# Performance work log

Hardware: AMD Instinct MI355X
Metric: run time of the kernel (lower is better)

The kernel has to match this reference:

```python
import jax, jax.numpy as jnp
import numpy as np

IN, H, OUT = 8, 256, 24  # input_size, hidden_size, output_size
B, T = 2048, 256


def _gate_step(hx, x, Wx, Wh, b):
    # Fused version of the 8 per-gate Linears: one [.,IN]@[IN,4H] + one [.,H]@[H,4H]
    gates = x @ Wx + hx @ Wh + b            # [B, 4H]
    i, f, o, g = jnp.split(gates, 4, axis=-1)
    i, f, o = jax.nn.sigmoid(i), jax.nn.sigmoid(f), jax.nn.sigmoid(o)
    g = jnp.tanh(g)
    # NOTE: in the original code cx is never reassigned, so it stays zeros and
    # cy = cx*f + i*g == i*g on every step. We replicate that exactly.
    cy = i * g
    return o * jnp.tanh(cy)


def setup_inputs() -> dict:
    key = jax.random.key(0)
    ks = jax.random.split(key, 9)
    s = 0.05
    return {
        "inputs0": jax.random.normal(ks[0], (B, T, IN), jnp.float32),
        "inputs1": jax.random.normal(ks[1], (B, OUT - 1), jnp.float32),
        # concatenated gate weights, order [i | f | o | c]
        "Wx": jax.random.normal(ks[2], (IN, 4 * H), jnp.float32) * s,
        "Wh": jax.random.normal(ks[3], (H, 4 * H), jnp.float32) * s,
        "b": jax.random.normal(ks[4], (4 * H,), jnp.float32) * s,  # bx + bh folded
        "Wy": jax.random.normal(ks[5], (H, 1), jnp.float32) * s,
        "by": jax.random.normal(ks[6], (1,), jnp.float32) * s,
        # fresh random Linear(1, IN) per decoder step in the original -> per-step params
        "dec_w": jax.random.normal(ks[7], (OUT - 1, IN), jnp.float32) * s,
        "dec_b": jax.random.normal(ks[8], (OUT - 1, IN), jnp.float32) * s,
    }


def reference(inputs0, inputs1, Wx, Wh, b, Wy, by, dec_w, dec_b):
    bsz = inputs0.shape[0]
    h0 = jnp.zeros((bsz, H), inputs0.dtype)

    # ---- encoder: scan over time (strict recurrence) ----
    x_seq = jnp.transpose(inputs0, (1, 0, 2))  # [T, B, IN]

    def enc_step(h, x):
        return _gate_step(h, x, Wx, Wh, b), None

    h, _ = jax.lax.scan(enc_step, h0, x_seq)
    hy0 = h @ Wy + by                           # [B, 1]

    # ---- decoder: OUT-1 steps, each with its own fresh 1->IN linear ----
    x1_seq = jnp.transpose(inputs1, (1, 0))[: OUT - 1]  # [OUT-1, B]

    def dec_step(h, inp):
        x1, w, bb = inp
        x = x1[:, None] * w[None, :] + bb[None, :]      # [B, IN]
        h = _gate_step(h, x, Wx, Wh, b)
        return h, h @ Wy + by                            # y: [B, 1]

    _, ys = jax.lax.scan(dec_step, h, (x1_seq, dec_w, dec_b))  # ys: [OUT-1, B, 1]

    hy = jnp.concatenate([hy0, jnp.transpose(ys[..., 0], (1, 0))], axis=1)  # [B, OUT]
    return hy
```

## Files before the change

### kernel.cpp

```cpp
#include <hip/hip_runtime.h>


typedef short bf16x8 __attribute__((ext_vector_type(8)));
typedef float f32x4 __attribute__((ext_vector_type(4)));

#define T_ENC 256
#define N_DEC 23
#define NSTEP 279
#define HSTR 296
#define REG_T 37
#define LDS_T 17
#define WPACK_SHORTS (48 * 9 * 512)

__device__ __forceinline__ short f2bf(float f) {
  unsigned u = __float_as_uint(f);
  u = (u + 0x7fffu + ((u >> 16) & 1u)) >> 16;
  return (short)u;
}
__device__ __forceinline__ float bf2f(short s) {
  return __uint_as_float(((unsigned)(unsigned short)s) << 16);
}

#if __has_builtin(__builtin_amdgcn_rcpf)
#define RCPF(x) __builtin_amdgcn_rcpf(x)
#else
#define RCPF(x) (1.0f / (x))
#endif

__device__ __forceinline__ float sigm(float x) { return RCPF(1.0f + __expf(-x)); }
__device__ __forceinline__ float tanhf_fast(float x) {
  return 1.0f - 2.0f * RCPF(__expf(2.0f * x) + 1.0f);
}

__global__ void pack_kernel(const float* __restrict__ Wx, const float* __restrict__ Wh,
                            const float* __restrict__ b, short* __restrict__ Wpack,
                            float* __restrict__ bpack) {
  int tau = blockIdx.x;
  int l = threadIdx.x;
  int n_tile = tau / 9, kt = tau % 9;
  int w = n_tile / 6, t = n_tile % 6;
  int gate = t >> 1, loc = t & 1;
  int base = (gate == 0) ? 0 : (gate == 1 ? 512 : 768);
  int c = l & 15, q = l >> 4;
  int oc = base + w * 32 + loc * 16 + c;
  bf16x8 v;
#pragma unroll
  for (int e = 0; e < 8; ++e) {
    int k = kt * 32 + q * 8 + e;
    float f;
    if (k < 256)      f = Wh[k * 1024 + oc];
    else if (k < 264) f = Wx[(k - 256) * 1024 + oc];
    else              f = 0.0f;
    v[e] = f2bf(f);
  }
  ((bf16x8*)Wpack)[tau * 64 + l] = v;
  if (kt == 0 && q == 0) bpack[n_tile * 16 + c] = b[oc];
}

__global__ __launch_bounds__(512, 2) void lstm_kernel(
    const float* __restrict__ inputs0, const float* __restrict__ inputs1,
    const float* __restrict__ Wy, const float* __restrict__ by,
    const float* __restrict__ dec_w, const float* __restrict__ dec_b,
    const short* __restrict__ Wpack, const float* __restrict__ bpack,
    float* __restrict__ out) {
  __shared__ short B_lds[8 * LDS_T * 512];
  __shared__ short hbuf[16 * HSTR];
  __shared__ float Wy_lds[256];
  __shared__ float ypart[256];

  const int tid = threadIdx.x;
  const int wg = blockIdx.x;
  const int lane = tid & 63;
  const int w = tid >> 6;
  const int q = lane >> 4;
  const int c = lane & 15;

  const bf16x8* wp = (const bf16x8*)Wpack;

  bf16x8 Breg[REG_T];
#pragma unroll
  for (int r = 0; r < REG_T; ++r) Breg[r] = wp[(w * 54 + r) * 64 + lane];

  for (int j = 0; j < LDS_T; ++j) {
    bf16x8 v = wp[(w * 54 + REG_T + j) * 64 + lane];
    *(bf16x8*)(B_lds + (w * LDS_T + j) * 512 + lane * 8) = v;
  }

  for (int i = tid; i < 16 * HSTR; i += 512) hbuf[i] = 0;
  if (tid < 256) Wy_lds[tid] = Wy[tid];
  __syncthreads();

  if (tid < 128) {
    int m = tid >> 3, kk = tid & 7;
    hbuf[m * HSTR + 256 + kk] = f2bf(inputs0[((wg * 16 + m) * 256 + 0) * 8 + kk]);
  }
  float bias[6];
#pragma unroll
  for (int t = 0; t < 6; ++t) bias[t] = bpack[w * 96 + t * 16 + c];
  const float byv = by[0];
  __syncthreads();

#define LDSB(j) (*(const bf16x8*)(B_lds + (w * LDS_T + (j)) * 512 + lane * 8))

  for (int s = 0; s < NSTEP; ++s) {
    bf16x8 A[9];
#pragma unroll
    for (int kt = 0; kt < 9; ++kt)
      A[kt] = *(const bf16x8*)(hbuf + c * HSTR + kt * 32 + q * 8);

    __syncthreads();

    float xv = 0.0f;
    const bool do_x = (tid < 128) && (s + 1 < NSTEP);
    const int xm = tid >> 3, xk = tid & 7;
    if (do_x) {
      int sn = s + 1;
      if (sn < T_ENC) {
        xv = inputs0[((wg * 16 + xm) * 256 + sn) * 8 + xk];
      } else {
        int d = sn - T_ENC;
        xv = inputs1[(wg * 16 + xm) * N_DEC + d] * dec_w[d * 8 + xk] + dec_b[d * 8 + xk];
      }
    }

    f32x4 acc[6];
#pragma unroll
    for (int t = 0; t < 6; ++t) {
      f32x4 a; a[0] = bias[t]; a[1] = bias[t]; a[2] = bias[t]; a[3] = bias[t];
      acc[t] = a;
    }
#pragma unroll
    for (int t = 0; t < 4; ++t)
#pragma unroll
      for (int kt = 0; kt < 9; ++kt)
        acc[t] = __builtin_amdgcn_mfma_f32_16x16x32_bf16(A[kt], Breg[t * 9 + kt], acc[t], 0, 0, 0);
    acc[4] = __builtin_amdgcn_mfma_f32_16x16x32_bf16(A[0], Breg[36], acc[4], 0, 0, 0);
#pragma unroll
    for (int j = 0; j < LDS_T; ++j) {
      const int t = (j < 8) ? 4 : 5;
      const int kt = (j < 8) ? (j + 1) : (j - 8);
      acc[t] = __builtin_amdgcn_mfma_f32_16x16x32_bf16(A[kt], LDSB(j), acc[t], 0, 0, 0);
    }

#pragma unroll
    for (int p = 0; p < 2; ++p) {
      f32x4 iv = acc[p], ov = acc[2 + p], gv = acc[4 + p];
#pragma unroll
      for (int r = 0; r < 4; ++r) {
        float ii = sigm(iv[r]);
        float oo = sigm(ov[r]);
        float gg = tanhf_fast(gv[r]);
        float h = oo * tanhf_fast(ii * gg);
        hbuf[(4 * q + r) * HSTR + (w * 32 + p * 16 + c)] = f2bf(h);
      }
    }
    if (do_x) hbuf[xm * HSTR + 256 + xk] = f2bf(xv);
    __syncthreads();

    if (s >= T_ENC - 1) {
      if (tid < 256) {
        int m = tid & 15, kq = tid >> 4;
        float part = 0.0f;
#pragma unroll
        for (int j = 0; j < 16; ++j)
          part += bf2f(hbuf[m * HSTR + kq * 16 + j]) * Wy_lds[kq * 16 + j];
        ypart[tid] = part;
      }
      __syncthreads();
      if (tid < 16) {
        float y = byv;
#pragma unroll
        for (int kq = 0; kq < 16; ++kq) y += ypart[kq * 16 + tid];
        out[(wg * 16 + tid) * 24 + (s - (T_ENC - 1))] = y;
      }
    }
  }
}

extern "C" void kernel_launch(void* const* d_in, const int* in_sizes, int n_in,
                              void* d_out, int out_size, void* d_ws, size_t ws_size,
                              hipStream_t stream) {
  const float* inputs0 = (const float*)d_in[0];
  const float* inputs1 = (const float*)d_in[1];
  const float* Wx      = (const float*)d_in[2];
  const float* Wh      = (const float*)d_in[3];
  const float* b       = (const float*)d_in[4];
  const float* Wy      = (const float*)d_in[5];
  const float* by      = (const float*)d_in[6];
  const float* dec_w   = (const float*)d_in[7];
  const float* dec_b   = (const float*)d_in[8];

  short* Wpack = (short*)d_ws;
  float* bpack = (float*)((char*)d_ws + WPACK_SHORTS * 2);

  pack_kernel<<<dim3(48 * 9), dim3(64), 0, stream>>>(Wx, Wh, b, Wpack, bpack);
  lstm_kernel<<<dim3(128), dim3(512), 0, stream>>>(
      inputs0, inputs1, Wy, by, dec_w, dec_b, Wpack, bpack, (float*)d_out);
}
```

Before: 530.0 us.

## Split batch into 8-row blocks over 256 workgroups, fold bias into GEMM

Each workgroup now handles 8 batch rows instead of 16, so twice as many workgroups run the recurrence and more CUs are busy. The A operand duplicates the 8 rows across the 16-row MFMA tile. The bias is folded into the GEMM as an extra K column holding a constant 1.0. More weight tiles are kept in registers (45 in registers, 9 in LDS), and the A fragments are streamed through a 3-deep rotating buffer during the MFMA loop. In exchange, half of each MFMA computes duplicate rows, the bias is rounded to bf16, and register pressure rises.

```diff
diff --git a/kernel.cpp b/kernel.cpp
--- a/kernel.cpp
+++ b/kernel.cpp
@@ -8,8 +8,8 @@
 #define N_DEC 23
 #define NSTEP 279
 #define HSTR 296
-#define REG_T 37
-#define LDS_T 17
+#define REG_T 45
+#define LDS_T 9
 #define WPACK_SHORTS (48 * 9 * 512)
 
 __device__ __forceinline__ short f2bf(float f) {
@@ -33,8 +33,7 @@
 }
 
 __global__ void pack_kernel(const float* __restrict__ Wx, const float* __restrict__ Wh,
-                            const float* __restrict__ b, short* __restrict__ Wpack,
-                            float* __restrict__ bpack) {
+                            const float* __restrict__ b, short* __restrict__ Wpack) {
   int tau = blockIdx.x;
   int l = threadIdx.x;
   int n_tile = tau / 9, kt = tau % 9;
@@ -48,25 +47,24 @@
   for (int e = 0; e < 8; ++e) {
     int k = kt * 32 + q * 8 + e;
     float f;
-    if (k < 256)      f = Wh[k * 1024 + oc];
-    else if (k < 264) f = Wx[(k - 256) * 1024 + oc];
-    else              f = 0.0f;
+    if (k < 256)       f = Wh[k * 1024 + oc];
+    else if (k < 264)  f = Wx[(k - 256) * 1024 + oc];
+    else if (k == 264) f = b[oc];
+    else               f = 0.0f;
     v[e] = f2bf(f);
   }
   ((bf16x8*)Wpack)[tau * 64 + l] = v;
-  if (kt == 0 && q == 0) bpack[n_tile * 16 + c] = b[oc];
 }
 
 __global__ __launch_bounds__(512, 2) void lstm_kernel(
     const float* __restrict__ inputs0, const float* __restrict__ inputs1,
     const float* __restrict__ Wy, const float* __restrict__ by,
     const float* __restrict__ dec_w, const float* __restrict__ dec_b,
-    const short* __restrict__ Wpack, const float* __restrict__ bpack,
-    float* __restrict__ out) {
-  __shared__ short B_lds[8 * LDS_T * 512];
-  __shared__ short hbuf[16 * HSTR];
+    const short* __restrict__ Wpack, float* __restrict__ out) {
+  __shared__ __align__(16) short B_lds[8 * LDS_T * 512];
+  __shared__ __align__(16) short hbuf[16 * HSTR];
   __shared__ float Wy_lds[256];
-  __shared__ float ypart[256];
+  __shared__ float ypart[128];
 
   const int tid = threadIdx.x;
   const int wg = blockIdx.x;
@@ -80,7 +78,7 @@
   bf16x8 Breg[REG_T];
 #pragma unroll
   for (int r = 0; r < REG_T; ++r) Breg[r] = wp[(w * 54 + r) * 64 + lane];
-
+#pragma unroll
   for (int j = 0; j < LDS_T; ++j) {
     bf16x8 v = wp[(w * 54 + REG_T + j) * 64 + lane];
     *(bf16x8*)(B_lds + (w * LDS_T + j) * 512 + lane * 8) = v;
@@ -90,88 +88,84 @@
   if (tid < 256) Wy_lds[tid] = Wy[tid];
   __syncthreads();
 
-  if (tid < 128) {
+  if (tid < 64) {
     int m = tid >> 3, kk = tid & 7;
-    hbuf[m * HSTR + 256 + kk] = f2bf(inputs0[((wg * 16 + m) * 256 + 0) * 8 + kk]);
+    hbuf[m * HSTR + 256 + kk] = f2bf(inputs0[((wg * 8 + m) * 256 + 0) * 8 + kk]);
   }
-  float bias[6];
-#pragma unroll
-  for (int t = 0; t < 6; ++t) bias[t] = bpack[w * 96 + t * 16 + c];
+  if (tid < 8) hbuf[tid * HSTR + 264] = (short)0x3F80;
   const float byv = by[0];
   __syncthreads();
 
+#define RDA(kt) (*(const bf16x8*)(hbuf + (c & 7) * HSTR + (kt) * 32 + q * 8))
 #define LDSB(j) (*(const bf16x8*)(B_lds + (w * LDS_T + (j)) * 512 + lane * 8))
 
   for (int s = 0; s < NSTEP; ++s) {
-    bf16x8 A[9];
-#pragma unroll
-    for (int kt = 0; kt < 9; ++kt)
-      A[kt] = *(const bf16x8*)(hbuf + c * HSTR + kt * 32 + q * 8);
-
-    __syncthreads();
-
     float xv = 0.0f;
-    const bool do_x = (tid < 128) && (s + 1 < NSTEP);
+    const bool do_x = (tid < 64) && (s + 1 < NSTEP);
     const int xm = tid >> 3, xk = tid & 7;
     if (do_x) {
       int sn = s + 1;
       if (sn < T_ENC) {
-        xv = inputs0[((wg * 16 + xm) * 256 + sn) * 8 + xk];
+        xv = inputs0[((wg * 8 + xm) * 256 + sn) * 8 + xk];
       } else {
         int d = sn - T_ENC;
-        xv = inputs1[(wg * 16 + xm) * N_DEC + d] * dec_w[d * 8 + xk] + dec_b[d * 8 + xk];
+        xv = inputs1[(wg * 8 + xm) * N_DEC + d] * dec_w[d * 8 + xk] + dec_b[d * 8 + xk];
       }
     }
 
+    bf16x8 A3[3];
+    A3[0] = RDA(0); A3[1] = RDA(1); A3[2] = RDA(2);
     f32x4 acc[6];
 #pragma unroll
-    for (int t = 0; t < 6; ++t) {
-      f32x4 a; a[0] = bias[t]; a[1] = bias[t]; a[2] = bias[t]; a[3] = bias[t];
-      acc[t] = a;
+    for (int t = 0; t < 6; ++t) { acc[t][0] = 0.f; acc[t][1] = 0.f; acc[t][2] = 0.f; acc[t][3] = 0.f; }
+#pragma unroll
+    for (int kt = 0; kt < 9; ++kt) {
+      const bf16x8 a = A3[kt % 3];
+#pragma unroll
+      for (int t = 0; t < 5; ++t)
+        acc[t] = __builtin_amdgcn_mfma_f32_16x16x32_bf16(a, Breg[t * 9 + kt], acc[t], 0, 0, 0);
+      acc[5] = __builtin_amdgcn_mfma_f32_16x16x32_bf16(a, LDSB(kt), acc[5], 0, 0, 0);
+      if (kt + 3 < 9) A3[kt % 3] = RDA(kt + 3);
     }
+    __syncthreads();
+
+    const int qh = q >> 1;
+    const f32x4 vi = qh ? acc[1] : acc[0];
+    const f32x4 vo = qh ? acc[3] : acc[2];
+    const f32x4 vg = qh ? acc[5] : acc[4];
+    const int row0 = (q & 1) * 4;
+    const int colw = w * 32 + qh * 16 + c;
 #pragma unroll
-    for (int t = 0; t < 4; ++t)
-#pragma unroll
-      for (int kt = 0; kt < 9; ++kt)
-        acc[t] = __builtin_amdgcn_mfma_f32_16x16x32_bf16(A[kt], Breg[t * 9 + kt], acc[t], 0, 0, 0);
-    acc[4] = __builtin_amdgcn_mfma_f32_16x16x32_bf16(A[0], Breg[36], acc[4], 0, 0, 0);
-#pragma unroll
-    for (int j = 0; j < LDS_T; ++j) {
-      const int t = (j < 8) ? 4 : 5;
-      const int kt = (j < 8) ? (j + 1) : (j - 8);
-      acc[t] = __builtin_amdgcn_mfma_f32_16x16x32_bf16(A[kt], LDSB(j), acc[t], 0, 0, 0);
-    }
-
-#pragma unroll
-    for (int p = 0; p < 2; ++p) {
-      f32x4 iv = acc[p], ov = acc[2 + p], gv = acc[4 + p];
-#pragma unroll
-      for (int r = 0; r < 4; ++r) {
-        float ii = sigm(iv[r]);
-        float oo = sigm(ov[r]);
-        float gg = tanhf_fast(gv[r]);
-        float h = oo * tanhf_fast(ii * gg);
-        hbuf[(4 * q + r) * HSTR + (w * 32 + p * 16 + c)] = f2bf(h);
-      }
+    for (int j = 0; j < 4; ++j) {
+      float ii = sigm(vi[j]);
+      float oo = sigm(vo[j]);
+      float gg = tanhf_fast(vg[j]);
+      float h = oo * tanhf_fast(ii * gg);
+      hbuf[(row0 + j) * HSTR + colw] = f2bf(h);
     }
     if (do_x) hbuf[xm * HSTR + 256 + xk] = f2bf(xv);
     __syncthreads();
 
     if (s >= T_ENC - 1) {
-      if (tid < 256) {
-        int m = tid & 15, kq = tid >> 4;
+      if (tid < 128) {
+        int m = tid & 7, kq = tid >> 3;
+        const short* hp = hbuf + m * HSTR + kq * 16;
+        bf16x8 h0 = *(const bf16x8*)(hp);
+        bf16x8 h1 = *(const bf16x8*)(hp + 8);
         float part = 0.0f;
 #pragma unroll
-        for (int j = 0; j < 16; ++j)
-          part += bf2f(hbuf[m * HSTR + kq * 16 + j]) * Wy_lds[kq * 16 + j];
+        for (int j = 0; j < 8; ++j) {
+          part += bf2f(h0[j]) * Wy_lds[kq * 16 + j];
+          part += bf2f(h1[j]) * Wy_lds[kq * 16 + 8 + j];
+        }
         ypart[tid] = part;
       }
       __syncthreads();
-      if (tid < 16) {
+      if (tid < 8) {
         float y = byv;
 #pragma unroll
-        for (int kq = 0; kq < 16; ++kq) y += ypart[kq * 16 + tid];
-        out[(wg * 16 + tid) * 24 + (s - (T_ENC - 1))] = y;
+        for (int kq = 0; kq < 16; ++kq) y += ypart[kq * 8 + tid];
+        out[(wg * 8 + tid) * 24 + (s - (T_ENC - 1))] = y;
       }
     }
   }
@@ -191,9 +185,8 @@
   const float* dec_b   = (const float*)d_in[8];
 
   short* Wpack = (short*)d_ws;
-  float* bpack = (float*)((char*)d_ws + WPACK_SHORTS * 2);
 
-  pack_kernel<<<dim3(48 * 9), dim3(64), 0, stream>>>(Wx, Wh, b, Wpack, bpack);
-  lstm_kernel<<<dim3(128), dim3(512), 0, stream>>>(
-      inputs0, inputs1, Wy, by, dec_w, dec_b, Wpack, bpack, (float*)d_out);
+  pack_kernel<<<dim3(48 * 9), dim3(64), 0, stream>>>(Wx, Wh, b, Wpack);
+  lstm_kernel<<<dim3(256), dim3(512), 0, stream>>>(
+      inputs0, inputs1, Wy, by, dec_w, dec_b, Wpack, (float*)d_out);
 }
```

Result: faster. 425.0 us (-19.8%).
